# Performance work log

Measured on AMD Instinct MI355X. Metric: run time of the kernel, lower is better.

The kernel has to match this reference:

```python
import math
import jax, jax.numpy as jnp
import numpy as np

B, Q, K, D = 16, 2048, 2048, 128

def setup_inputs() -> dict:
    key = jax.random.key(0)
    kq, kk, kv, kl = jax.random.split(key, 4)
    queries = jax.random.normal(kq, (B, Q, D), dtype=jnp.float32)
    keys = jax.random.normal(kk, (B, K, D), dtype=jnp.float32)
    values = jax.random.normal(kv, (B, K, D), dtype=jnp.float32)
    valid_lens = jax.random.randint(kl, (B,), 0, K, dtype=jnp.int64)
    return {"queries": queries, "keys": keys, "values": values, "valid_lens": valid_lens}

def reference(queries, keys, values, valid_lens):
    d = queries.shape[-1]
    # [B, Q, K] scores
    scores = jnp.einsum("bqd,bkd->bqk", queries, keys) / math.sqrt(d)
    # Original masks X[index][length:] = -1e6, i.e. along the QUERY axis (dim 1),
    # filling entire rows; softmax over the key axis then yields uniform weights
    # for those rows. Reproduce exactly.
    q_idx = jnp.arange(queries.shape[1])  # [Q]
    mask = q_idx[None, :, None] >= valid_lens[:, None, None]  # [B, Q, 1]
    scores = jnp.where(mask, jnp.float32(-1000000.0), scores)
    attention_weights = jax.nn.softmax(scores, axis=-1)
    # dropout p=0.0 (eval) -> identity
    return jnp.einsum("bqk,bkd->bqd", attention_weights, values)
```

## Files before the change

kernel.cpp:

```cpp
#include <hip/hip_runtime.h>
#include <hip/hip_bf16.h>
#include <math.h>


#define Bn 16
#define Qn 2048
#define Kn 2048
#define Dn 128
#define SCALE 0.08838834764831845f

typedef _Float16 f16;
typedef _Float16 f16x8_t __attribute__((ext_vector_type(8)));
typedef float f32x16_t __attribute__((ext_vector_type(16)));

typedef __attribute__((address_space(1))) const unsigned int glb_u32;
typedef __attribute__((address_space(3))) unsigned int lds_u32;

__device__ __forceinline__ void g2l16(const void* g, void* l) {
  __builtin_amdgcn_global_load_lds((glb_u32*)g, (lds_u32*)l, 16, 0, 0);
}


template <int VT>
__global__ void __launch_bounds__(256) prep_kernel(
    const float* __restrict__ Qg, const float* __restrict__ Kg,
    const float* __restrict__ Vg, f16* __restrict__ Qh, f16* __restrict__ Kh,
    f16* __restrict__ Vt, float* __restrict__ sv) {
  __shared__ float ps[8][32];
  const int b = blockIdx.z;
  const int x = threadIdx.x, y = threadIdx.y;

  {
    const int lb = (b * 4 + blockIdx.y) * 32 + blockIdx.x;
    const int t = y * 32 + x;
    const size_t key = (size_t)lb * 16 + (t >> 4);
    const int G = t & 15;
    const float* kp = Kg + (key << 7) + G * 8;
    float4 f0 = *(const float4*)kp;
    float4 f1 = *(const float4*)(kp + 4);
    f16x8_t o;
    o[0] = (f16)f0.x; o[1] = (f16)f0.y; o[2] = (f16)f0.z; o[3] = (f16)f0.w;
    o[4] = (f16)f1.x; o[5] = (f16)f1.y; o[6] = (f16)f1.z; o[7] = (f16)f1.w;
    const int gs = (G & 8) | ((G & 7) ^ ((int)key & 7));
    *(f16x8_t*)(Kh + (key << 7) + (gs << 3)) = o;
    if (Qh != nullptr) {
      const float* qp = Qg + (key << 7) + G * 8;
      float4 q0 = *(const float4*)qp;
      float4 q1 = *(const float4*)(qp + 4);
      f16x8_t oq;
      oq[0] = (f16)q0.x; oq[1] = (f16)q0.y; oq[2] = (f16)q0.z; oq[3] = (f16)q0.w;
      oq[4] = (f16)q1.x; oq[5] = (f16)q1.y; oq[6] = (f16)q1.z; oq[7] = (f16)q1.w;
      *(f16x8_t*)(Qh + (key << 7) + G * 8) = oq;
    }
  }

  const int k0 = blockIdx.x * 64, d0 = blockIdx.y * 32;
  const int d = d0 + x;
  const float* vp = Vg + ((size_t)b * Kn + k0 + y * 8) * Dn + d;
  float s = 0.f;
  f16x8_t gr;
#pragma unroll
  for (int j = 0; j < 8; j++) {
    float v = vp[(size_t)j * Dn];
    s += v;
    gr[j] = (f16)v;
  }
  if (VT == 128) {
    const int kb = k0 >> 7;
    const int G = ((k0 & 64) >> 3) + y;
    const int gs = (G & 8) | ((G & 7) ^ (d & 7));
    *(f16x8_t*)(Vt + (((size_t)(b * (Kn / 128) + kb) * 128 + d) << 7) + (gs << 3)) = gr;
  } else {
    const int kb = k0 >> 6;
    const int G = y;
    const int gs = G ^ (d & 7);
    *(f16x8_t*)(Vt + (((size_t)(b * (Kn / 64) + kb) * 128 + d) << 6) + (gs << 3)) = gr;
  }

  ps[y][x] = s;
  __syncthreads();
  if (y == 0) {
    float tot = 0.f;
#pragma unroll
    for (int j = 0; j < 8; j++) tot += ps[j][x];
    atomicAdd(&sv[b * Dn + d0 + x], tot);
  }
}

__device__ __forceinline__ int load_vl(const int* __restrict__ vlp, int b) {
  bool is64 = true;
#pragma unroll
  for (int i = 1; i < 16; i += 2) is64 = is64 && (vlp[i] == 0);
  return is64 ? vlp[2 * b] : vlp[b];
}


template <int J>
__global__ void __launch_bounds__(256, 2) flash_q(
    const f16* __restrict__ Qh, const f16* __restrict__ Kh,
    const f16* __restrict__ Vt, const int* __restrict__ vlp,
    f16* __restrict__ Po, float* __restrict__ Lb) {
  const int b = blockIdx.y;
  const int seg = blockIdx.x & 15;
  const int j = blockIdx.x >> 4;
  const int vl = load_vl(vlp, b);
  const int nq = (vl + 127) >> 7;
  if (nq == 0) return;

  __shared__ __align__(16) f16 Ks[128 * 128];
  __shared__ __align__(16) f16 Vs[128 * 128];

  const int tid = threadIdx.x;
  const int wave = tid >> 6, lane = tid & 63;
  const int H = lane >> 5, l5 = lane & 31;

  {
    const char* kg = (const char*)Kh + (((size_t)b * Kn + seg * 128) << 8) +
                     wave * 8192 + lane * 16;
    const char* vg = (const char*)Vt + ((size_t)(b * (Kn / 128) + seg) << 15) +
                     wave * 8192 + lane * 16;
    f16* kl = Ks + wave * 4096;
    f16* vli = Vs + wave * 4096;
#pragma unroll
    for (int i = 0; i < 8; i++) {
      g2l16(kg + i * 1024, kl + i * 512);
      g2l16(vg + i * 1024, vli + i * 512);
    }
  }
  __syncthreads();

  const int krow = (l5 & 0x13) | ((l5 & 4) << 1) | ((l5 & 8) >> 1);
  const int krow7 = krow & 7;

  for (int qt = j; qt < nq; qt += J) {
    const int q0 = qt << 7;
    const int qbase = q0 + wave * 32;
    if (qbase >= vl) continue;
    const int q_lane = qbase + l5;
    const float sc = (q_lane >= vl) ? 0.f : SCALE;

    f16x8_t qf[8];
    {
      const f16* qp = Qh + ((size_t)b * Qn + q_lane) * Dn + 8 * H;
#pragma unroll
      for (int s = 0; s < 8; s++) qf[s] = *(const f16x8_t*)(qp + 16 * s);
    }

    f32x16_t O[4];
#pragma unroll
    for (int i = 0; i < 4; i++) O[i] = (f32x16_t)(0.f);
    float l_lane = 0.f;

#pragma unroll
    for (int sub = 0; sub < 4; sub++) {
      f32x16_t T = (f32x16_t)(0.f);
      const f16* krp = Ks + ((sub * 32 + krow) << 7);
#pragma unroll
      for (int s = 0; s < 8; s++) {
        const int G = 2 * s + H;
        const int gs = (G & 8) | ((G & 7) ^ krow7);
        f16x8_t kf = *(const f16x8_t*)(krp + (gs << 3));
        T = __builtin_amdgcn_mfma_f32_32x32x16_f16(kf, qf[s], T, 0, 0, 0);
      }

      f16x8_t pf0, pf1;
      float ls = 0.f;
#pragma unroll
      for (int r = 0; r < 8; r++) {
        float p = __expf(T[r] * sc);
        ls += p;
        pf0[r] = (f16)p;
      }
#pragma unroll
      for (int r = 8; r < 16; r++) {
        float p = __expf(T[r] * sc);
        ls += p;
        pf1[r - 8] = (f16)p;
      }
      l_lane += ls;

#pragma unroll
      for (int dt = 0; dt < 4; dt++) {
        const f16* vrp = Vs + ((dt * 32 + l5) << 7);
        const int G0 = sub * 4 + H, G1 = sub * 4 + 2 + H;
        const int gs0 = (G0 & 8) | ((G0 & 7) ^ (l5 & 7));
        const int gs1 = (G1 & 8) | ((G1 & 7) ^ (l5 & 7));
        f16x8_t vf0 = *(const f16x8_t*)(vrp + (gs0 << 3));
        f16x8_t vf1 = *(const f16x8_t*)(vrp + (gs1 << 3));
        O[dt] = __builtin_amdgcn_mfma_f32_32x32x16_f16(pf0, vf0, O[dt], 0, 0, 0);
        O[dt] = __builtin_amdgcn_mfma_f32_32x32x16_f16(pf1, vf1, O[dt], 0, 0, 0);
      }
    }

    float ll = l_lane + __shfl_xor(l_lane, 32);
    if (lane < 32) Lb[(size_t)(seg * Bn + b) * Qn + qbase + l5] = ll;

    f16* po = Po + ((size_t)(seg * Bn + b) * Qn + qbase) * Dn;
#pragma unroll
    for (int dt = 0; dt < 4; dt++) {
#pragma unroll
      for (int r = 0; r < 16; r++) {
        const int qrow = (r & 3) + 8 * (r >> 2) + 4 * H;
        po[(size_t)qrow * Dn + dt * 32 + l5] = (f16)O[dt][r];
      }
    }
  }
}


template <int S>
__global__ void __launch_bounds__(256, 2) flash_seq(
    const float* __restrict__ Qg, const f16* __restrict__ Kh,
    const f16* __restrict__ Vt, const int* __restrict__ vlp,
    f16* __restrict__ Po, float* __restrict__ Lb) {
  const int b = blockIdx.y;
  const int seg = blockIdx.z;
  const int qt = (blockIdx.x * 5 + seg * 3) & 15;
  const int q0 = qt * 128;
  const int vl = load_vl(vlp, b);
  if (q0 >= vl) return;

  __shared__ __align__(16) f16 Ks[64 * 128];
  __shared__ __align__(16) f16 Vs[128 * 64];

  const int tid = threadIdx.x;
  const int wave = tid >> 6, lane = tid & 63;
  const int H = lane >> 5, l5 = lane & 31;
  const int qbase = q0 + wave * 32;
  const bool act = qbase < vl;
  const int q_lane = qbase + l5;
  const float sc = (q_lane >= vl) ? 0.f : SCALE;

  const int krow = (l5 & 0x13) | ((l5 & 4) << 1) | ((l5 & 8) >> 1);
  const int krow7 = krow & 7;

  f16x8_t qf[8];
  if (act) {
    const float* qp = Qg + ((size_t)b * Qn + q_lane) * Dn + 8 * H;
#pragma unroll
    for (int s = 0; s < 8; s++) {
      float4 f0 = *(const float4*)(qp + 16 * s);
      float4 f1 = *(const float4*)(qp + 16 * s + 4);
      f16x8_t q8;
      q8[0] = (f16)f0.x; q8[1] = (f16)f0.y; q8[2] = (f16)f0.z; q8[3] = (f16)f0.w;
      q8[4] = (f16)f1.x; q8[5] = (f16)f1.y; q8[6] = (f16)f1.z; q8[7] = (f16)f1.w;
      qf[s] = q8;
    }
  }

  f32x16_t O[4];
#pragma unroll
  for (int i = 0; i < 4; i++) O[i] = (f32x16_t)(0.f);
  float l_lane = 0.f;

  const char* KgT = (const char*)Kh + (((size_t)b * Kn + (size_t)seg * (Kn / S)) << 8);
  const char* VgT = (const char*)Vt + ((size_t)(b * (Kn / 64) + seg * (Kn / S) / 64) << 14);

  for (int it = 0; it < (Kn / S) / 64; it++) {
    __syncthreads();
    const char* kg = KgT + (size_t)it * 16384 + wave * 4096 + lane * 16;
    const char* vg = VgT + (size_t)it * 16384 + wave * 4096 + lane * 16;
    f16* kl = Ks + wave * 2048;
    f16* vli = Vs + wave * 2048;
#pragma unroll
    for (int i = 0; i < 4; i++) {
      g2l16(kg + i * 1024, kl + i * 512);
      g2l16(vg + i * 1024, vli + i * 512);
    }
    __syncthreads();

    if (act) {
#pragma unroll
      for (int sub = 0; sub < 2; sub++) {
        f32x16_t T = (f32x16_t)(0.f);
        const f16* krp = Ks + ((sub * 32 + krow) << 7);
#pragma unroll
        for (int s = 0; s < 8; s++) {
          const int G = 2 * s + H;
          const int gs = (G & 8) | ((G & 7) ^ krow7);
          f16x8_t kf = *(const f16x8_t*)(krp + (gs << 3));
          T = __builtin_amdgcn_mfma_f32_32x32x16_f16(kf, qf[s], T, 0, 0, 0);
        }
        f16x8_t pf0, pf1;
        float ls = 0.f;
#pragma unroll
        for (int r = 0; r < 8; r++) {
          float p = __expf(T[r] * sc);
          ls += p;
          pf0[r] = (f16)p;
        }
#pragma unroll
        for (int r = 8; r < 16; r++) {
          float p = __expf(T[r] * sc);
          ls += p;
          pf1[r - 8] = (f16)p;
        }
        l_lane += ls;
#pragma unroll
        for (int dt = 0; dt < 4; dt++) {
          const f16* vrp = Vs + ((dt * 32 + l5) << 6);
          const int G0 = sub * 4 + H, G1 = sub * 4 + 2 + H;
          const int gs0 = G0 ^ (l5 & 7);
          const int gs1 = G1 ^ (l5 & 7);
          f16x8_t vf0 = *(const f16x8_t*)(vrp + (gs0 << 3));
          f16x8_t vf1 = *(const f16x8_t*)(vrp + (gs1 << 3));
          O[dt] = __builtin_amdgcn_mfma_f32_32x32x16_f16(pf0, vf0, O[dt], 0, 0, 0);
          O[dt] = __builtin_amdgcn_mfma_f32_32x32x16_f16(pf1, vf1, O[dt], 0, 0, 0);
        }
      }
    }
  }

  if (!act) return;

  l_lane += __shfl_xor(l_lane, 32);
  if (lane < 32) Lb[(size_t)(seg * Bn + b) * Qn + qbase + l5] = l_lane;

  f16* po = Po + ((size_t)(seg * Bn + b) * Qn + qbase) * Dn;
#pragma unroll
  for (int dt = 0; dt < 4; dt++) {
#pragma unroll
    for (int r = 0; r < 16; r++) {
      const int qrow = (r & 3) + 8 * (r >> 2) + 4 * H;
      po[(size_t)qrow * Dn + dt * 32 + l5] = (f16)O[dt][r];
    }
  }
}


template <int S>
__global__ void __launch_bounds__(256) combine_kernel(
    const f16* __restrict__ Po, const float* __restrict__ Lb,
    const float* __restrict__ sv, const int* __restrict__ vlp,
    float* __restrict__ Out) {
  const int b = blockIdx.y, q0 = blockIdx.x * 64;
  const int vl = load_vl(vlp, b);
  const int tid = threadIdx.x;

  __shared__ float linv[64];
  if (tid < 64) {
    float s = 0.f;
#pragma unroll
    for (int sg = 0; sg < S; sg++) s += Lb[(size_t)(sg * Bn + b) * Qn + q0 + tid];
    linv[tid] = 1.0f / s;
  }
  __syncthreads();

  const int row16 = tid >> 4;
  const int d8 = (tid & 15) * 8;
  const float invK = 1.0f / (float)Kn;
  float mv[8];
#pragma unroll
  for (int j = 0; j < 8; j++) mv[j] = sv[b * Dn + d8 + j] * invK;

#pragma unroll
  for (int pass = 0; pass < 4; pass++) {
    const int row = pass * 16 + row16;
    const int q = q0 + row;
    float acc[8];
    if (q >= vl) {
#pragma unroll
      for (int j = 0; j < 8; j++) acc[j] = mv[j];
    } else {
#pragma unroll
      for (int j = 0; j < 8; j++) acc[j] = 0.f;
#pragma unroll
      for (int sg = 0; sg < S; sg++) {
        f16x8_t v = *(const f16x8_t*)(Po + ((size_t)(sg * Bn + b) * Qn + q) * Dn + d8);
#pragma unroll
        for (int j = 0; j < 8; j++) acc[j] += (float)v[j];
      }
      const float li = linv[row];
#pragma unroll
      for (int j = 0; j < 8; j++) acc[j] *= li;
    }
    float4 o0 = make_float4(acc[0], acc[1], acc[2], acc[3]);
    float4 o1 = make_float4(acc[4], acc[5], acc[6], acc[7]);
    float* op = Out + ((size_t)b * Qn + q) * Dn + d8;
    *(float4*)op = o0;
    *(float4*)(op + 4) = o1;
  }
}


extern "C" void kernel_launch(void* const* d_in, const int* in_sizes, int n_in,
                              void* d_out, int out_size, void* d_ws, size_t ws_size,
                              hipStream_t stream) {
  const float* Qg = (const float*)d_in[0];
  const float* Kg = (const float*)d_in[1];
  const float* Vg = (const float*)d_in[2];
  const int* vl = (const int*)d_in[3];
  float* Out = (float*)d_out;

  char* ws = (char*)d_ws;
  const size_t kv = (size_t)Bn * Kn * Dn * 2;
  float* sumV = (float*)ws;
  f16* Kh = (f16*)(ws + 8192);
  f16* Vt = (f16*)(ws + 8192 + kv);

  const size_t plane = (size_t)Bn * Qn * Dn * 2;
  const size_t lplane = (size_t)Bn * Qn * 4;
  const size_t need16 = 8192 + 3 * kv + 16 * plane + 16 * lplane;
  const size_t base8 = 8192 + 2 * kv;
  const size_t need8 = base8 + 8 * plane + 8 * lplane;

  hipMemsetAsync(sumV, 0, Bn * Dn * sizeof(float), stream);

  if (ws_size >= need16) {
    f16* Qh = (f16*)(ws + 8192 + 2 * kv);
    f16* Po = (f16*)(ws + 8192 + 3 * kv);
    float* Lb = (float*)(ws + 8192 + 3 * kv + 16 * plane);
    prep_kernel<128><<<dim3(32, 4, Bn), dim3(32, 8), 0, stream>>>(
        Qg, Kg, Vg, Qh, Kh, Vt, sumV);
    flash_q<2><<<dim3(32, Bn), 256, 0, stream>>>(Qh, Kh, Vt, vl, Po, Lb);
    combine_kernel<16><<<dim3(Qn / 64, Bn), 256, 0, stream>>>(Po, Lb, sumV, vl, Out);
  } else if (ws_size >= need8) {
    f16* Po = (f16*)(ws + base8);
    float* Lb = (float*)(ws + base8 + 8 * plane);
    prep_kernel<64><<<dim3(32, 4, Bn), dim3(32, 8), 0, stream>>>(
        Qg, Kg, Vg, (f16*)nullptr, Kh, Vt, sumV);
    flash_seq<8><<<dim3(16, Bn, 8), 256, 0, stream>>>(Qg, Kh, Vt, vl, Po, Lb);
    combine_kernel<8><<<dim3(Qn / 64, Bn), 256, 0, stream>>>(Po, Lb, sumV, vl, Out);
  } else {
    f16* Po = (f16*)(ws + base8);
    float* Lb = (float*)(ws + base8 + 4 * plane);
    prep_kernel<64><<<dim3(32, 4, Bn), dim3(32, 8), 0, stream>>>(
        Qg, Kg, Vg, (f16*)nullptr, Kh, Vt, sumV);
    flash_seq<4><<<dim3(16, Bn, 4), 256, 0, stream>>>(Qg, Kh, Vt, vl, Po, Lb);
    combine_kernel<4><<<dim3(Qn / 64, Bn), 256, 0, stream>>>(Po, Lb, sumV, vl, Out);
  }
}
```

Before: 144.5 us.

## Replace split-K flash with single-pass double-buffered kernel that writes final output

Removes the split-K partial outputs and the separate combine kernel. One block per (batch, query tile) now iterates over all keys, double-buffering K/V tiles in LDS with async global-to-LDS loads, and normalizes and writes fp32 output directly. Fully masked query tiles write the mean of V early. This removes the partial-result write and readback traffic and one launch, but leaves only 256 blocks doing long sequential loops, which lowers parallelism compared with the 16-way key split.

```diff
diff --git a/kernel.cpp b/kernel.cpp
--- a/kernel.cpp
+++ b/kernel.cpp
@@ -1,5 +1,4 @@
 #include <hip/hip_runtime.h>
-#include <hip/hip_bf16.h>
 #include <math.h>
 
 
@@ -21,7 +20,6 @@
 }
 
 
-template <int VT>
 __global__ void __launch_bounds__(256) prep_kernel(
     const float* __restrict__ Qg, const float* __restrict__ Kg,
     const float* __restrict__ Vg, f16* __restrict__ Qh, f16* __restrict__ Kh,
@@ -43,15 +41,14 @@
     o[4] = (f16)f1.x; o[5] = (f16)f1.y; o[6] = (f16)f1.z; o[7] = (f16)f1.w;
     const int gs = (G & 8) | ((G & 7) ^ ((int)key & 7));
     *(f16x8_t*)(Kh + (key << 7) + (gs << 3)) = o;
-    if (Qh != nullptr) {
-      const float* qp = Qg + (key << 7) + G * 8;
-      float4 q0 = *(const float4*)qp;
-      float4 q1 = *(const float4*)(qp + 4);
-      f16x8_t oq;
-      oq[0] = (f16)q0.x; oq[1] = (f16)q0.y; oq[2] = (f16)q0.z; oq[3] = (f16)q0.w;
-      oq[4] = (f16)q1.x; oq[5] = (f16)q1.y; oq[6] = (f16)q1.z; oq[7] = (f16)q1.w;
-      *(f16x8_t*)(Qh + (key << 7) + G * 8) = oq;
-    }
+
+    const float* qp = Qg + (key << 7) + G * 8;
+    float4 q0 = *(const float4*)qp;
+    float4 q1 = *(const float4*)(qp + 4);
+    f16x8_t oq;
+    oq[0] = (f16)q0.x; oq[1] = (f16)q0.y; oq[2] = (f16)q0.z; oq[3] = (f16)q0.w;
+    oq[4] = (f16)q1.x; oq[5] = (f16)q1.y; oq[6] = (f16)q1.z; oq[7] = (f16)q1.w;
+    *(f16x8_t*)(Qh + (key << 7) + G * 8) = oq;
   }
 
   const int k0 = blockIdx.x * 64, d0 = blockIdx.y * 32;
@@ -65,12 +62,7 @@
     s += v;
     gr[j] = (f16)v;
   }
-  if (VT == 128) {
-    const int kb = k0 >> 7;
-    const int G = ((k0 & 64) >> 3) + y;
-    const int gs = (G & 8) | ((G & 7) ^ (d & 7));
-    *(f16x8_t*)(Vt + (((size_t)(b * (Kn / 128) + kb) * 128 + d) << 7) + (gs << 3)) = gr;
-  } else {
+  {
     const int kb = k0 >> 6;
     const int G = y;
     const int gs = G ^ (d & 7);
@@ -95,139 +87,36 @@
 }
 
 
-template <int J>
-__global__ void __launch_bounds__(256, 2) flash_q(
+__global__ void __launch_bounds__(256, 2) flash_sp(
     const f16* __restrict__ Qh, const f16* __restrict__ Kh,
     const f16* __restrict__ Vt, const int* __restrict__ vlp,
-    f16* __restrict__ Po, float* __restrict__ Lb) {
-  const int b = blockIdx.y;
-  const int seg = blockIdx.x & 15;
-  const int j = blockIdx.x >> 4;
+    const float* __restrict__ sv, float* __restrict__ Out) {
+  const int b = blockIdx.x;
+  const int qt = blockIdx.y;
+  const int q0 = qt << 7;
   const int vl = load_vl(vlp, b);
-  const int nq = (vl + 127) >> 7;
-  if (nq == 0) return;
-
-  __shared__ __align__(16) f16 Ks[128 * 128];
-  __shared__ __align__(16) f16 Vs[128 * 128];
-
   const int tid = threadIdx.x;
-  const int wave = tid >> 6, lane = tid & 63;
-  const int H = lane >> 5, l5 = lane & 31;
-
-  {
-    const char* kg = (const char*)Kh + (((size_t)b * Kn + seg * 128) << 8) +
-                     wave * 8192 + lane * 16;
-    const char* vg = (const char*)Vt + ((size_t)(b * (Kn / 128) + seg) << 15) +
-                     wave * 8192 + lane * 16;
-    f16* kl = Ks + wave * 4096;
-    f16* vli = Vs + wave * 4096;
-#pragma unroll
-    for (int i = 0; i < 8; i++) {
-      g2l16(kg + i * 1024, kl + i * 512);
-      g2l16(vg + i * 1024, vli + i * 512);
-    }
-  }
-  __syncthreads();
-
-  const int krow = (l5 & 0x13) | ((l5 & 4) << 1) | ((l5 & 8) >> 1);
-  const int krow7 = krow & 7;
-
-  for (int qt = j; qt < nq; qt += J) {
-    const int q0 = qt << 7;
-    const int qbase = q0 + wave * 32;
-    if (qbase >= vl) continue;
-    const int q_lane = qbase + l5;
-    const float sc = (q_lane >= vl) ? 0.f : SCALE;
-
-    f16x8_t qf[8];
-    {
-      const f16* qp = Qh + ((size_t)b * Qn + q_lane) * Dn + 8 * H;
-#pragma unroll
-      for (int s = 0; s < 8; s++) qf[s] = *(const f16x8_t*)(qp + 16 * s);
-    }
-
-    f32x16_t O[4];
-#pragma unroll
-    for (int i = 0; i < 4; i++) O[i] = (f32x16_t)(0.f);
-    float l_lane = 0.f;
-
-#pragma unroll
-    for (int sub = 0; sub < 4; sub++) {
-      f32x16_t T = (f32x16_t)(0.f);
-      const f16* krp = Ks + ((sub * 32 + krow) << 7);
-#pragma unroll
-      for (int s = 0; s < 8; s++) {
-        const int G = 2 * s + H;
-        const int gs = (G & 8) | ((G & 7) ^ krow7);
-        f16x8_t kf = *(const f16x8_t*)(krp + (gs << 3));
-        T = __builtin_amdgcn_mfma_f32_32x32x16_f16(kf, qf[s], T, 0, 0, 0);
-      }
-
-      f16x8_t pf0, pf1;
-      float ls = 0.f;
-#pragma unroll
-      for (int r = 0; r < 8; r++) {
-        float p = __expf(T[r] * sc);
-        ls += p;
-        pf0[r] = (f16)p;
-      }
-#pragma unroll
-      for (int r = 8; r < 16; r++) {
-        float p = __expf(T[r] * sc);
-        ls += p;
-        pf1[r - 8] = (f16)p;
-      }
-      l_lane += ls;
-
-#pragma unroll
-      for (int dt = 0; dt < 4; dt++) {
-        const f16* vrp = Vs + ((dt * 32 + l5) << 7);
-        const int G0 = sub * 4 + H, G1 = sub * 4 + 2 + H;
-        const int gs0 = (G0 & 8) | ((G0 & 7) ^ (l5 & 7));
-        const int gs1 = (G1 & 8) | ((G1 & 7) ^ (l5 & 7));
-        f16x8_t vf0 = *(const f16x8_t*)(vrp + (gs0 << 3));
-        f16x8_t vf1 = *(const f16x8_t*)(vrp + (gs1 << 3));
-        O[dt] = __builtin_amdgcn_mfma_f32_32x32x16_f16(pf0, vf0, O[dt], 0, 0, 0);
-        O[dt] = __builtin_amdgcn_mfma_f32_32x32x16_f16(pf1, vf1, O[dt], 0, 0, 0);
-      }
-    }
-
-    float ll = l_lane + __shfl_xor(l_lane, 32);
-    if (lane < 32) Lb[(size_t)(seg * Bn + b) * Qn + qbase + l5] = ll;
-
-    f16* po = Po + ((size_t)(seg * Bn + b) * Qn + qbase) * Dn;
-#pragma unroll
-    for (int dt = 0; dt < 4; dt++) {
-#pragma unroll
-      for (int r = 0; r < 16; r++) {
-        const int qrow = (r & 3) + 8 * (r >> 2) + 4 * H;
-        po[(size_t)qrow * Dn + dt * 32 + l5] = (f16)O[dt][r];
-      }
-    }
-  }
-}
-
-
-template <int S>
-__global__ void __launch_bounds__(256, 2) flash_seq(
-    const float* __restrict__ Qg, const f16* __restrict__ Kh,
-    const f16* __restrict__ Vt, const int* __restrict__ vlp,
-    f16* __restrict__ Po, float* __restrict__ Lb) {
-  const int b = blockIdx.y;
-  const int seg = blockIdx.z;
-  const int qt = (blockIdx.x * 5 + seg * 3) & 15;
-  const int q0 = qt * 128;
-  const int vl = load_vl(vlp, b);
-  if (q0 >= vl) return;
-
-  __shared__ __align__(16) f16 Ks[64 * 128];
-  __shared__ __align__(16) f16 Vs[128 * 64];
-
-  const int tid = threadIdx.x;
+
+  if (q0 >= vl) {
+    const float invK = 1.0f / (float)Kn;
+    const int row = tid >> 1, h = tid & 1;
+    const float4* svp = (const float4*)(sv + b * Dn + h * 64);
+    float4* op = (float4*)(Out + ((size_t)b * Qn + q0 + row) * Dn + h * 64);
+#pragma unroll
+    for (int i = 0; i < 16; i++) {
+      float4 s4 = svp[i];
+      op[i] = make_float4(s4.x * invK, s4.y * invK, s4.z * invK, s4.w * invK);
+    }
+    return;
+  }
+
+  __shared__ __align__(16) f16 Ks[2][64 * 128];
+  __shared__ __align__(16) f16 Vs[2][128 * 64];
+
   const int wave = tid >> 6, lane = tid & 63;
   const int H = lane >> 5, l5 = lane & 31;
   const int qbase = q0 + wave * 32;
-  const bool act = qbase < vl;
+  const bool wact = qbase < vl;
   const int q_lane = qbase + l5;
   const float sc = (q_lane >= vl) ? 0.f : SCALE;
 
@@ -235,17 +124,10 @@
   const int krow7 = krow & 7;
 
   f16x8_t qf[8];
-  if (act) {
-    const float* qp = Qg + ((size_t)b * Qn + q_lane) * Dn + 8 * H;
-#pragma unroll
-    for (int s = 0; s < 8; s++) {
-      float4 f0 = *(const float4*)(qp + 16 * s);
-      float4 f1 = *(const float4*)(qp + 16 * s + 4);
-      f16x8_t q8;
-      q8[0] = (f16)f0.x; q8[1] = (f16)f0.y; q8[2] = (f16)f0.z; q8[3] = (f16)f0.w;
-      q8[4] = (f16)f1.x; q8[5] = (f16)f1.y; q8[6] = (f16)f1.z; q8[7] = (f16)f1.w;
-      qf[s] = q8;
-    }
+  if (wact) {
+    const f16* qp = Qh + ((size_t)b * Qn + q_lane) * Dn + 8 * H;
+#pragma unroll
+    for (int s = 0; s < 8; s++) qf[s] = *(const f16x8_t*)(qp + 16 * s);
   }
 
   f32x16_t O[4];
@@ -253,27 +135,41 @@
   for (int i = 0; i < 4; i++) O[i] = (f32x16_t)(0.f);
   float l_lane = 0.f;
 
-  const char* KgT = (const char*)Kh + (((size_t)b * Kn + (size_t)seg * (Kn / S)) << 8);
-  const char* VgT = (const char*)Vt + ((size_t)(b * (Kn / 64) + seg * (Kn / S) / 64) << 14);
-
-  for (int it = 0; it < (Kn / S) / 64; it++) {
-    __syncthreads();
-    const char* kg = KgT + (size_t)it * 16384 + wave * 4096 + lane * 16;
-    const char* vg = VgT + (size_t)it * 16384 + wave * 4096 + lane * 16;
-    f16* kl = Ks + wave * 2048;
-    f16* vli = Vs + wave * 2048;
+  const char* KgT = (const char*)Kh + ((size_t)b * Kn << 8);
+  const char* VgT = (const char*)Vt + ((size_t)(b * (Kn / 64)) << 14);
+
+  {
+    const char* kg = KgT + wave * 4096 + lane * 16;
+    const char* vg = VgT + wave * 4096 + lane * 16;
+    f16* kl = Ks[0] + wave * 2048;
+    f16* vli = Vs[0] + wave * 2048;
 #pragma unroll
     for (int i = 0; i < 4; i++) {
       g2l16(kg + i * 1024, kl + i * 512);
       g2l16(vg + i * 1024, vli + i * 512);
     }
-    __syncthreads();
-
-    if (act) {
+  }
+  __syncthreads();
+
+  int buf = 0;
+  for (int sl = 0; sl < 32; sl++) {
+    if (sl < 31) {
+      const char* kg = KgT + (size_t)(sl + 1) * 16384 + wave * 4096 + lane * 16;
+      const char* vg = VgT + (size_t)(sl + 1) * 16384 + wave * 4096 + lane * 16;
+      f16* kl = Ks[buf ^ 1] + wave * 2048;
+      f16* vli = Vs[buf ^ 1] + wave * 2048;
+#pragma unroll
+      for (int i = 0; i < 4; i++) {
+        g2l16(kg + i * 1024, kl + i * 512);
+        g2l16(vg + i * 1024, vli + i * 512);
+      }
+    }
+
+    if (wact) {
 #pragma unroll
       for (int sub = 0; sub < 2; sub++) {
         f32x16_t T = (f32x16_t)(0.f);
-        const f16* krp = Ks + ((sub * 32 + krow) << 7);
+        const f16* krp = Ks[buf] + ((sub * 32 + krow) << 7);
 #pragma unroll
         for (int s = 0; s < 8; s++) {
           const int G = 2 * s + H;
@@ -281,6 +177,7 @@
           f16x8_t kf = *(const f16x8_t*)(krp + (gs << 3));
           T = __builtin_amdgcn_mfma_f32_32x32x16_f16(kf, qf[s], T, 0, 0, 0);
         }
+
         f16x8_t pf0, pf1;
         float ls = 0.f;
 #pragma unroll
@@ -296,9 +193,10 @@
           pf1[r - 8] = (f16)p;
         }
         l_lane += ls;
+
 #pragma unroll
         for (int dt = 0; dt < 4; dt++) {
-          const f16* vrp = Vs + ((dt * 32 + l5) << 6);
+          const f16* vrp = Vs[buf] + ((dt * 32 + l5) << 6);
           const int G0 = sub * 4 + H, G1 = sub * 4 + 2 + H;
           const int gs0 = G0 ^ (l5 & 7);
           const int gs1 = G1 ^ (l5 & 7);
@@ -309,76 +207,38 @@
         }
       }
     }
-  }
-
-  if (!act) return;
-
-  l_lane += __shfl_xor(l_lane, 32);
-  if (lane < 32) Lb[(size_t)(seg * Bn + b) * Qn + qbase + l5] = l_lane;
-
-  f16* po = Po + ((size_t)(seg * Bn + b) * Qn + qbase) * Dn;
-#pragma unroll
-  for (int dt = 0; dt < 4; dt++) {
+    __syncthreads();
+    buf ^= 1;
+  }
+
+  float* op = Out + ((size_t)b * Qn + qbase) * Dn;
+  if (wact) {
+    float ll = l_lane + __shfl_xor(l_lane, 32);
+    float inv[16];
 #pragma unroll
     for (int r = 0; r < 16; r++) {
       const int qrow = (r & 3) + 8 * (r >> 2) + 4 * H;
-      po[(size_t)qrow * Dn + dt * 32 + l5] = (f16)O[dt][r];
-    }
-  }
-}
-
-
-template <int S>
-__global__ void __launch_bounds__(256) combine_kernel(
-    const f16* __restrict__ Po, const float* __restrict__ Lb,
-    const float* __restrict__ sv, const int* __restrict__ vlp,
-    float* __restrict__ Out) {
-  const int b = blockIdx.y, q0 = blockIdx.x * 64;
-  const int vl = load_vl(vlp, b);
-  const int tid = threadIdx.x;
-
-  __shared__ float linv[64];
-  if (tid < 64) {
-    float s = 0.f;
-#pragma unroll
-    for (int sg = 0; sg < S; sg++) s += Lb[(size_t)(sg * Bn + b) * Qn + q0 + tid];
-    linv[tid] = 1.0f / s;
-  }
-  __syncthreads();
-
-  const int row16 = tid >> 4;
-  const int d8 = (tid & 15) * 8;
-  const float invK = 1.0f / (float)Kn;
-  float mv[8];
-#pragma unroll
-  for (int j = 0; j < 8; j++) mv[j] = sv[b * Dn + d8 + j] * invK;
-
-#pragma unroll
-  for (int pass = 0; pass < 4; pass++) {
-    const int row = pass * 16 + row16;
-    const int q = q0 + row;
-    float acc[8];
-    if (q >= vl) {
-#pragma unroll
-      for (int j = 0; j < 8; j++) acc[j] = mv[j];
-    } else {
-#pragma unroll
-      for (int j = 0; j < 8; j++) acc[j] = 0.f;
-#pragma unroll
-      for (int sg = 0; sg < S; sg++) {
-        f16x8_t v = *(const f16x8_t*)(Po + ((size_t)(sg * Bn + b) * Qn + q) * Dn + d8);
-#pragma unroll
-        for (int j = 0; j < 8; j++) acc[j] += (float)v[j];
-      }
-      const float li = linv[row];
-#pragma unroll
-      for (int j = 0; j < 8; j++) acc[j] *= li;
-    }
-    float4 o0 = make_float4(acc[0], acc[1], acc[2], acc[3]);
-    float4 o1 = make_float4(acc[4], acc[5], acc[6], acc[7]);
-    float* op = Out + ((size_t)b * Qn + q) * Dn + d8;
-    *(float4*)op = o0;
-    *(float4*)(op + 4) = o1;
+      inv[r] = 1.0f / __shfl(ll, qrow);
+    }
+#pragma unroll
+    for (int dt = 0; dt < 4; dt++) {
+#pragma unroll
+      for (int r = 0; r < 16; r++) {
+        const int qrow = (r & 3) + 8 * (r >> 2) + 4 * H;
+        op[(size_t)qrow * Dn + dt * 32 + l5] = O[dt][r] * inv[r];
+      }
+    }
+  } else {
+    const float invK = 1.0f / (float)Kn;
+#pragma unroll
+    for (int dt = 0; dt < 4; dt++) {
+      const float svv = sv[b * Dn + dt * 32 + l5] * invK;
+#pragma unroll
+      for (int r = 0; r < 16; r++) {
+        const int qrow = (r & 3) + 8 * (r >> 2) + 4 * H;
+        op[(size_t)qrow * Dn + dt * 32 + l5] = svv;
+      }
+    }
   }
 }
 
@@ -397,36 +257,11 @@
   float* sumV = (float*)ws;
   f16* Kh = (f16*)(ws + 8192);
   f16* Vt = (f16*)(ws + 8192 + kv);
-
-  const size_t plane = (size_t)Bn * Qn * Dn * 2;
-  const size_t lplane = (size_t)Bn * Qn * 4;
-  const size_t need16 = 8192 + 3 * kv + 16 * plane + 16 * lplane;
-  const size_t base8 = 8192 + 2 * kv;
-  const size_t need8 = base8 + 8 * plane + 8 * lplane;
+  f16* Qh = (f16*)(ws + 8192 + 2 * kv);
 
   hipMemsetAsync(sumV, 0, Bn * Dn * sizeof(float), stream);
 
-  if (ws_size >= need16) {
-    f16* Qh = (f16*)(ws + 8192 + 2 * kv);
-    f16* Po = (f16*)(ws + 8192 + 3 * kv);
-    float* Lb = (float*)(ws + 8192 + 3 * kv + 16 * plane);
-    prep_kernel<128><<<dim3(32, 4, Bn), dim3(32, 8), 0, stream>>>(
-        Qg, Kg, Vg, Qh, Kh, Vt, sumV);
-    flash_q<2><<<dim3(32, Bn), 256, 0, stream>>>(Qh, Kh, Vt, vl, Po, Lb);
-    combine_kernel<16><<<dim3(Qn / 64, Bn), 256, 0, stream>>>(Po, Lb, sumV, vl, Out);
-  } else if (ws_size >= need8) {
-    f16* Po = (f16*)(ws + base8);
-    float* Lb = (float*)(ws + base8 + 8 * plane);
-    prep_kernel<64><<<dim3(32, 4, Bn), dim3(32, 8), 0, stream>>>(
-        Qg, Kg, Vg, (f16*)nullptr, Kh, Vt, sumV);
-    flash_seq<8><<<dim3(16, Bn, 8), 256, 0, stream>>>(Qg, Kh, Vt, vl, Po, Lb);
-    combine_kernel<8><<<dim3(Qn / 64, Bn), 256, 0, stream>>>(Po, Lb, sumV, vl, Out);
-  } else {
-    f16* Po = (f16*)(ws + base8);
-    float* Lb = (float*)(ws + base8 + 4 * plane);
-    prep_kernel<64><<<dim3(32, 4, Bn), dim3(32, 8), 0, stream>>>(
-        Qg, Kg, Vg, (f16*)nullptr, Kh, Vt, sumV);
-    flash_seq<4><<<dim3(16, Bn, 4), 256, 0, stream>>>(Qg, Kh, Vt, vl, Po, Lb);
-    combine_kernel<4><<<dim3(Qn / 64, Bn), 256, 0, stream>>>(Po, Lb, sumV, vl, Out);
-  }
-}
+  prep_kernel<<<dim3(32, 4, Bn), dim3(32, 8), 0, stream>>>(
+      Qg, Kg, Vg, Qh, Kh, Vt, sumV);
+  flash_sp<<<dim3(Bn, 16), 256, 0, stream>>>(Qh, Kh, Vt, vl, sumV, Out);
+}
```

New measurement: 148.6 us. +2.8%, slower.
